# Kernel optimization log

Hardware: AMD Instinct MI355X
Metric: run time of the kernel (lower is better)

Reference implementation:

```python
import jax, jax.numpy as jnp
import numpy as np

N, K, C_S, C_Z, C_G, N_RBF = 1024, 16, 256, 128, 16, 64
EPS = 1e-8


def _ln(x, g, b, eps=1e-5):
    m = x.mean(-1, keepdims=True)
    v = jnp.mean((x - m) ** 2, -1, keepdims=True)
    return (x - m) * jax.lax.rsqrt(v + eps) * g + b


def _rbf(D, D_count=N_RBF, D_min=0.0, D_max=20.0):
    mu = jnp.linspace(D_min, D_max, D_count, dtype=D.dtype)
    sigma = (D_max - D_min) / D_count
    return jnp.exp(-(((D[..., None] - mu) / sigma) ** 2))


def setup_inputs() -> dict:
    key = jax.random.key(0)
    ks = jax.random.split(key, 20)
    node_features = jax.random.normal(ks[0], (N, C_S), jnp.float32)
    trans = jax.random.normal(ks[1], (N, 3), jnp.float32) * 5.0  # CA translations, Angstrom-ish
    edge_features = jax.random.normal(ks[2], (N * K, C_Z), jnp.float32)
    # sparse graph laid out as K neighbors per node: dst = node i repeated K times
    src = jax.random.randint(ks[3], (N * K,), 0, N)
    dst = jnp.repeat(jnp.arange(N), K)
    edge_index = jnp.stack([src, dst]).astype(jnp.int64)
    batch = jnp.zeros((N,), jnp.int64)
    res_mask = jnp.ones((N,), bool)
    w = lambda k, i, o: jax.random.normal(k, (i, o), jnp.float32) * 0.02
    return {
        "node_features": node_features, "trans": trans, "edge_features": edge_features,
        "ln_g": jnp.ones((C_Z,), jnp.float32), "ln_b": jnp.zeros((C_Z,), jnp.float32),
        "Wl": w(ks[4], C_S, C_G), "bl": jnp.zeros((C_G,), jnp.float32),
        "Wr": w(ks[5], C_S, C_G), "br": jnp.zeros((C_G,), jnp.float32),
        "Wep": w(ks[6], C_Z, C_Z), "bep": jnp.zeros((C_Z,), jnp.float32),
        "Weg": w(ks[7], C_Z, C_Z), "beg": jnp.zeros((C_Z,), jnp.float32),
        "Wdg": w(ks[8], C_G * C_G, C_Z), "bdg": jnp.zeros((C_Z,), jnp.float32),
        "Wdp": w(ks[9], N_RBF, C_Z), "bdp": jnp.zeros((C_Z,), jnp.float32),
        "lno_g": jnp.ones((C_Z,), jnp.float32), "lno_b": jnp.zeros((C_Z,), jnp.float32),
        "Wout": w(ks[10], C_Z, C_Z), "bout": jnp.zeros((C_Z,), jnp.float32),
        "Wog": w(ks[11], C_Z, C_Z), "bog": jnp.zeros((C_Z,), jnp.float32),
        "edge_index": edge_index, "batch": batch, "res_mask": res_mask,
    }


def reference(node_features, trans, edge_features, ln_g, ln_b, Wl, bl, Wr, br,
              Wep, bep, Weg, beg, Wdg, bdg, Wdp, bdp, lno_g, lno_b, Wout, bout,
              Wog, bog, edge_index, batch, res_mask):
    n = node_features.shape[0]
    src = edge_index[0].reshape(n, K)              # neighbor indices per node [N,K]
    # sparse -> kNN: edges are grouped K per destination node
    knn_feats = edge_features.reshape(n, K, C_Z)
    knn_mask = res_mask[src] & res_mask[:, None]   # [N,K]
    z = _ln(knn_feats, ln_g, ln_b)
    # outer-product node gating
    nl = node_features @ Wl + bl                   # [N,c_g]
    nr = node_features @ Wr + br
    a = nl[src]                                    # [N,K,c_g]
    b = nr[src]
    edge3 = a[:, :, None, :, None] * b[:, None, :, None, :]   # [N,K,K,c_g,c_g]
    gate3 = edge3.reshape(n, K, K, C_G * C_G) @ Wdg + bdg     # [N,K,K,c_z]
    # RBF distance features among the K neighbors of each node
    t = trans[src]                                 # [N,K,3]
    d = jnp.linalg.norm(t[:, :, None, :] - t[:, None, :, :] + EPS, axis=-1)  # [N,K,K]
    df = _rbf(d) @ Wdp + bdp                       # [N,K,K,c_z]
    m2 = (knn_mask[:, :, None] & knn_mask[:, None, :]).astype(df.dtype)
    e3 = jax.nn.sigmoid(gate3) * df * m2[..., None]
    # gated edge projection
    e2 = jax.nn.sigmoid(z @ Weg + beg) * (z @ Wep + bep)      # [N,K,c_z]
    # triangle matmul: per channel c, [K,K] @ [K]
    upd = jnp.einsum('njkc,nkc->njc', e3, e2)                 # [N,K,c_z]
    upd = _ln(upd, lno_g, lno_b) @ Wout + bout
    upd = upd * jax.nn.sigmoid(z @ Wog + bog)
    # kNN -> sparse scatter back (masked)
    out = (upd * knn_mask[..., None].astype(upd.dtype)).reshape(n * K, C_Z)
    return out
```

## Files before the change

kernel.cpp:

```cpp
#include <hip/hip_runtime.h>
#include <hip/hip_bf16.h>
#include <math.h>

#define KNN  16
#define CZ   128
#define CG   16
#define CS   256
#define NRBF 64
#define NN   1024

typedef __attribute__((ext_vector_type(8))) _Float16 half8;
typedef __attribute__((ext_vector_type(2))) _Float16 half2v;
typedef __attribute__((ext_vector_type(4))) float f4_t;

#define MFMA_F16(A, B, C) __builtin_amdgcn_mfma_f32_16x16x32_f16((A), (B), (C), 0, 0, 0)

union U8 { half2v h[4]; half8 v; };

__device__ __forceinline__ half2v pk2(float x, float y) {
    auto t = __builtin_amdgcn_cvt_pkrtz(x, y);
    half2v r;
    __builtin_memcpy(&r, &t, 4);
    return r;
}
__device__ __forceinline__ float sig_(float x) {
    return __builtin_amdgcn_rcpf(1.0f + __expf(-x));
}

__global__ __launch_bounds__(256) void repack_kernel(
    const float* __restrict__ Wdp, const float* __restrict__ Wdg,
    const float* __restrict__ Wout, const float* __restrict__ Wep,
    const float* __restrict__ Weg, const float* __restrict__ Wog,
    _Float16* __restrict__ dst_base) {
    int gid = blockIdx.x * 256 + threadIdx.x;
    const float* src;
    int o;
    if (gid < 8192)        { src = Wdp;  o = gid; }
    else if (gid < 40960)  { src = Wdg;  o = gid - 8192; }
    else if (gid < 57344)  { src = Wout; o = gid - 40960; }
    else if (gid < 73728)  { src = Wep;  o = gid - 57344; }
    else if (gid < 90112)  { src = Weg;  o = gid - 73728; }
    else                   { src = Wog;  o = gid - 90112; }
    int t  = o & 7;
    int l  = (o >> 3) & 63;
    int ct = (o >> 9) & 7;
    int s  = o >> 12;
    int row = s * 32 + (l >> 4) * 8 + t;
    int col = ct * 16 + (l & 15);
    dst_base[gid] = (_Float16)src[row * CZ + col];
}

__global__ __launch_bounds__(64) void nlr_kernel(
    const float* __restrict__ nf,
    const float* __restrict__ Wl, const float* __restrict__ bl,
    const float* __restrict__ Wr, const float* __restrict__ br,
    float* __restrict__ nl, float* __restrict__ nr) {
    int n = blockIdx.x;
    int lane = threadIdx.x;
    int p = lane & 15, seg = lane >> 4;
    float accl = (seg == 0) ? bl[p] : 0.0f;
    float accr = (seg == 0) ? br[p] : 0.0f;
    const float* row = nf + n * CS + seg * 64;
    for (int i = 0; i < 64; ++i) {
        float v = row[i];
        int s = seg * 64 + i;
        accl += v * Wl[s * CG + p];
        accr += v * Wr[s * CG + p];
    }
    accl += __shfl_xor(accl, 16); accl += __shfl_xor(accl, 32);
    accr += __shfl_xor(accr, 16); accr += __shfl_xor(accr, 32);
    if (lane < 16) { nl[n * CG + lane] = accl; nr[n * CG + lane] = accr; }
}

__global__ __launch_bounds__(256) void edge_kernel(
    const float* __restrict__ ef,
    const float* __restrict__ lng, const float* __restrict__ lnb,
    const float* __restrict__ bep, const float* __restrict__ beg,
    const float* __restrict__ bog,
    const _Float16* __restrict__ Wepp,
    const _Float16* __restrict__ Wegp,
    const _Float16* __restrict__ Wogp,
    const int* __restrict__ src, const int* __restrict__ resmask,
    float* __restrict__ e2ws, float* __restrict__ ggws) {
    __shared__ _Float16 s_z[16][136];
    __shared__ float s_km[16];
    int n = blockIdx.x;
    int tid = threadIdx.x;
    if (tid < 16) {
        int sv = src[n * KNN + tid];
        s_km[tid] = (resmask[sv] != 0 && resmask[n] != 0) ? 1.0f : 0.0f;
    }
    int r = tid >> 4, seg = tid & 15;
    const float* row = ef + ((size_t)n * KNN + r) * CZ + seg * 8;
    f4_t x0 = *(const f4_t*)row;
    f4_t x1 = *(const f4_t*)(row + 4);
    float s = x0.x + x0.y + x0.z + x0.w + x1.x + x1.y + x1.z + x1.w;
    float q = x0.x * x0.x + x0.y * x0.y + x0.z * x0.z + x0.w * x0.w
            + x1.x * x1.x + x1.y * x1.y + x1.z * x1.z + x1.w * x1.w;
    #pragma unroll
    for (int m = 1; m < 16; m <<= 1) { s += __shfl_xor(s, m); q += __shfl_xor(q, m); }
    float mean = s * (1.0f / CZ);
    float var  = q * (1.0f / CZ) - mean * mean;
    float rs   = __builtin_amdgcn_rsqf(var + 1e-5f);
    int col = seg * 8;
    f4_t g0 = *(const f4_t*)(lng + col), g1 = *(const f4_t*)(lng + col + 4);
    f4_t b0 = *(const f4_t*)(lnb + col), b1 = *(const f4_t*)(lnb + col + 4);
    U8 zu;
    zu.h[0] = pk2((x0.x - mean) * rs * g0.x + b0.x, (x0.y - mean) * rs * g0.y + b0.y);
    zu.h[1] = pk2((x0.z - mean) * rs * g0.z + b0.z, (x0.w - mean) * rs * g0.w + b0.w);
    zu.h[2] = pk2((x1.x - mean) * rs * g1.x + b1.x, (x1.y - mean) * rs * g1.y + b1.y);
    zu.h[3] = pk2((x1.z - mean) * rs * g1.z + b1.z, (x1.w - mean) * rs * g1.w + b1.w);
    *(half8*)&s_z[r][col] = zu.v;
    __syncthreads();

    int wv = tid >> 6, lane = tid & 63, l15 = lane & 15, quad = lane >> 4;
    half8 A[4];
    #pragma unroll
    for (int st = 0; st < 4; ++st)
        A[st] = *(const half8*)&s_z[l15][st * 32 + quad * 8];

    #pragma unroll
    for (int cc = 0; cc < 2; ++cc) {
        int ct = wv * 2 + cc;
        int c = ct * 16 + l15;
        float vep = bep[c], veg = beg[c], vog = bog[c];
        f4_t aep = {vep, vep, vep, vep};
        f4_t aeg = {veg, veg, veg, veg};
        f4_t aog = {vog, vog, vog, vog};
        #pragma unroll
        for (int st = 0; st < 4; ++st) {
            int off = ((st * 8 + ct) * 64 + lane) * 8;
            half8 bep_ = *(const half8*)(Wepp + off);
            half8 beg_ = *(const half8*)(Wegp + off);
            half8 bog_ = *(const half8*)(Wogp + off);
            aep = MFMA_F16(A[st], bep_, aep);
            aeg = MFMA_F16(A[st], beg_, aeg);
            aog = MFMA_F16(A[st], bog_, aog);
        }
        #pragma unroll
        for (int rr = 0; rr < 4; ++rr) {
            int er = quad * 4 + rr;
            size_t idx = ((size_t)n * KNN + er) * CZ + c;
            e2ws[idx] = sig_(aeg[rr]) * aep[rr] * s_km[er];
            ggws[idx] = sig_(aog[rr]);
        }
    }
}

__global__ __launch_bounds__(256) void main_kernel(
    const float* __restrict__ trans,
    const float* __restrict__ nl, const float* __restrict__ nr,
    const _Float16* __restrict__ Wdgp, const float* __restrict__ bdg,
    const _Float16* __restrict__ Wdpp, const float* __restrict__ bdp,
    const float* __restrict__ e2ws, const float* __restrict__ ggws,
    const float* __restrict__ lnog, const float* __restrict__ lnob,
    const _Float16* __restrict__ Woutp, const float* __restrict__ bout,
    const int* __restrict__ src, const int* __restrict__ resmask,
    float* __restrict__ out) {
    __shared__ float s_t[16 * 4];
    __shared__ float s_km[16];
    __shared__ int   s_src[16];
    __shared__ half2v s_a2[256];
    __shared__ float s_b[16 * 20];
    __shared__ float s_upd[16 * CZ];
    __shared__ _Float16 s_uln[16 * 136];

    int n = blockIdx.x;
    int tid = threadIdx.x;
    if (tid < 16) {
        int sv = src[n * KNN + tid];
        s_src[tid] = sv;
        s_km[tid] = (resmask[sv] != 0 && resmask[n] != 0) ? 1.0f : 0.0f;
        s_t[tid * 4 + 0] = trans[sv * 3 + 0];
        s_t[tid * 4 + 1] = trans[sv * 3 + 1];
        s_t[tid * 4 + 2] = trans[sv * 3 + 2];
    }
    __syncthreads();
    {
        int j = tid >> 4, p = tid & 15;
        int sv = s_src[j];
        float a = nl[sv * CG + p];
        s_a2[j * 16 + p] = pk2(a, a);
        s_b[j * 20 + p] = nr[sv * CG + p];
    }
    __syncthreads();

    int wv = tid >> 6, lane = tid & 63, l15 = lane & 15, quad = lane >> 4;

    half8 Bdg[8][2], Bdp[2][2];
    #pragma unroll
    for (int st = 0; st < 8; ++st)
        #pragma unroll
        for (int cc = 0; cc < 2; ++cc)
            Bdg[st][cc] = *(const half8*)(Wdgp + ((st * 8 + wv * 2 + cc) * 64 + lane) * 8);
    #pragma unroll
    for (int st = 0; st < 2; ++st)
        #pragma unroll
        for (int cc = 0; cc < 2; ++cc)
            Bdp[st][cc] = *(const half8*)(Wdpp + ((st * 8 + wv * 2 + cc) * 64 + lane) * 8);

    f4_t e2f[2];
    float bdgv[2], bdpv[2];
    #pragma unroll
    for (int cc = 0; cc < 2; ++cc) {
        int c = (wv * 2 + cc) * 16 + l15;
        bdgv[cc] = bdg[c];
        bdpv[cc] = bdp[c];
        #pragma unroll
        for (int rr = 0; rr < 4; ++rr)
            e2f[cc][rr] = e2ws[(size_t)(n * KNN + quad * 4 + rr) * CZ + c];
    }

    float tkx = s_t[l15 * 4 + 0], tky = s_t[l15 * 4 + 1], tkz = s_t[l15 * 4 + 2];
    f4_t bv0 = *(const f4_t*)&s_b[l15 * 20 + (quad & 1) * 8];
    f4_t bv1 = *(const f4_t*)&s_b[l15 * 20 + (quad & 1) * 8 + 4];
    half2v bh[4];
    bh[0] = pk2(bv0.x, bv0.y);
    bh[1] = pk2(bv0.z, bv0.w);
    bh[2] = pk2(bv1.x, bv1.y);
    bh[3] = pk2(bv1.z, bv1.w);
    int ph = quad >> 1;
    const float MUS = 20.0f / 63.0f;
    const float ISG = 1.0f / 0.3125f;
    float rIS[2];
    #pragma unroll
    for (int st = 0; st < 2; ++st)
        rIS[st] = (float)(st * 32 + quad * 8) * (MUS * ISG);

    for (int j = 0; j < 16; ++j) {
        float dx = s_t[j * 4 + 0] - tkx + 1e-8f;
        float dy = s_t[j * 4 + 1] - tky + 1e-8f;
        float dz = s_t[j * 4 + 2] - tkz + 1e-8f;
        float dI = sqrtf(dx * dx + dy * dy + dz * dz) * ISG;

        half8 ar[2];
        #pragma unroll
        for (int st = 0; st < 2; ++st) {
            U8 cv;
            float base0 = dI - rIS[st];
            #pragma unroll
            for (int tt = 0; tt < 4; ++tt) {
                float u0 = base0 - (float)(2 * tt) * (MUS * ISG);
                float u1 = u0 - (MUS * ISG);
                cv.h[tt] = pk2(__expf(-u0 * u0), __expf(-u1 * u1));
            }
            ar[st] = cv.v;
        }
        f4_t accd[2];
        #pragma unroll
        for (int cc = 0; cc < 2; ++cc) {
            f4_t z = {bdpv[cc], bdpv[cc], bdpv[cc], bdpv[cc]};
            z = MFMA_F16(ar[0], Bdp[0][cc], z);
            z = MFMA_F16(ar[1], Bdp[1][cc], z);
            accd[cc] = z;
        }

        f4_t accg[2];
        accg[0] = (f4_t){bdgv[0], bdgv[0], bdgv[0], bdgv[0]};
        accg[1] = (f4_t){bdgv[1], bdgv[1], bdgv[1], bdgv[1]};
        #pragma unroll
        for (int st = 0; st < 8; ++st) {
            half2v av = s_a2[j * 16 + st * 2 + ph];
            U8 ev;
            ev.h[0] = av * bh[0];
            ev.h[1] = av * bh[1];
            ev.h[2] = av * bh[2];
            ev.h[3] = av * bh[3];
            accg[0] = MFMA_F16(ev.v, Bdg[st][0], accg[0]);
            accg[1] = MFMA_F16(ev.v, Bdg[st][1], accg[1]);
        }

        float kmj = s_km[j];
        #pragma unroll
        for (int cc = 0; cc < 2; ++cc) {
            float part = 0.f;
            #pragma unroll
            for (int rr = 0; rr < 4; ++rr)
                part += sig_(accg[cc][rr]) * accd[cc][rr] * e2f[cc][rr];
            part += __shfl_xor(part, 16);
            part += __shfl_xor(part, 32);
            if (lane < 16) s_upd[j * CZ + (wv * 2 + cc) * 16 + lane] = part * kmj;
        }
    }
    __syncthreads();

    for (int rr = 0; rr < 4; ++rr) {
        int r = wv * 4 + rr;
        float x0 = s_upd[r * CZ + lane];
        float x1 = s_upd[r * CZ + 64 + lane];
        float sm = x0 + x1, sq = x0 * x0 + x1 * x1;
        #pragma unroll
        for (int m = 1; m < 64; m <<= 1) {
            sm += __shfl_xor(sm, m);
            sq += __shfl_xor(sq, m);
        }
        float mean = sm * (1.0f / CZ);
        float var  = sq * (1.0f / CZ) - mean * mean;
        float rsv  = __builtin_amdgcn_rsqf(var + 1e-5f);
        float h0 = (x0 - mean) * rsv * lnog[lane] + lnob[lane];
        float h1 = (x1 - mean) * rsv * lnog[64 + lane] + lnob[64 + lane];
        s_uln[r * 136 + lane]      = (_Float16)h0;
        s_uln[r * 136 + 64 + lane] = (_Float16)h1;
    }
    __syncthreads();

    half8 Aw[4];
    #pragma unroll
    for (int st = 0; st < 4; ++st)
        Aw[st] = *(const half8*)&s_uln[l15 * 136 + st * 32 + quad * 8];
    #pragma unroll
    for (int cc = 0; cc < 2; ++cc) {
        int c = (wv * 2 + cc) * 16 + l15;
        float bo = bout[c];
        f4_t acc = {bo, bo, bo, bo};
        #pragma unroll
        for (int st = 0; st < 4; ++st) {
            half8 bw = *(const half8*)(Woutp + ((st * 8 + wv * 2 + cc) * 64 + lane) * 8);
            acc = MFMA_F16(Aw[st], bw, acc);
        }
        #pragma unroll
        for (int rr = 0; rr < 4; ++rr) {
            int row = quad * 4 + rr;
            size_t oi = (size_t)(n * KNN + row) * CZ + c;
            out[oi] = acc[rr] * ggws[oi] * s_km[row];
        }
    }
}

extern "C" void kernel_launch(void* const* d_in, const int* in_sizes, int n_in,
                              void* d_out, int out_size, void* d_ws, size_t ws_size,
                              hipStream_t stream) {
    const float* node_features = (const float*)d_in[0];
    const float* trans         = (const float*)d_in[1];
    const float* edge_features = (const float*)d_in[2];
    const float* ln_g  = (const float*)d_in[3];
    const float* ln_b  = (const float*)d_in[4];
    const float* Wl    = (const float*)d_in[5];
    const float* bl    = (const float*)d_in[6];
    const float* Wr    = (const float*)d_in[7];
    const float* br    = (const float*)d_in[8];
    const float* Wep   = (const float*)d_in[9];
    const float* bep   = (const float*)d_in[10];
    const float* Weg   = (const float*)d_in[11];
    const float* beg   = (const float*)d_in[12];
    const float* Wdg   = (const float*)d_in[13];
    const float* bdg   = (const float*)d_in[14];
    const float* Wdp   = (const float*)d_in[15];
    const float* bdp   = (const float*)d_in[16];
    const float* lno_g = (const float*)d_in[17];
    const float* lno_b = (const float*)d_in[18];
    const float* Wout  = (const float*)d_in[19];
    const float* bout  = (const float*)d_in[20];
    const float* Wog   = (const float*)d_in[21];
    const float* bog   = (const float*)d_in[22];
    const int* edge_index = (const int*)d_in[23];
    const int* resmask    = (const int*)d_in[25];

    float* ws = (float*)d_ws;
    float* nl   = ws;
    float* nr   = nl + NN * CG;
    float* e2ws = nr + NN * CG;
    float* ggws = e2ws + (size_t)NN * KNN * CZ;
    _Float16* pk = (_Float16*)(ggws + (size_t)NN * KNN * CZ);
    _Float16* Wdpp  = pk;
    _Float16* Wdgp  = pk + 8192;
    _Float16* Woutp = pk + 40960;
    _Float16* Wepp  = pk + 57344;
    _Float16* Wegp  = pk + 73728;
    _Float16* Wogp  = pk + 90112;
    const int* src = edge_index;

    repack_kernel<<<416, 256, 0, stream>>>(Wdp, Wdg, Wout, Wep, Weg, Wog, pk);
    nlr_kernel<<<NN, 64, 0, stream>>>(node_features, Wl, bl, Wr, br, nl, nr);
    edge_kernel<<<NN, 256, 0, stream>>>(
        edge_features, ln_g, ln_b, bep, beg, bog, Wepp, Wegp, Wogp,
        src, resmask, e2ws, ggws);
    main_kernel<<<NN, 256, 0, stream>>>(
        trans, nl, nr, Wdgp, bdg, Wdpp, bdp, e2ws, ggws, lno_g, lno_b,
        Woutp, bout, src, resmask, (float*)d_out);
}
```

Before: 170.5 us.

## Fuse edge projections into main kernel and factor gate matmul through per-node tensor

Merges the weight repack and node-projection kernels into one prep launch, and folds the edge LayerNorm and gated projections into the main kernel so the e2 and gate intermediates stay in registers instead of round-tripping through global workspace. The 256-wide outer-product gate matmul is refactored: a per-node tensor T = a·Wdg (reshaped) is precomputed with 16x16x16 MFMAs into LDS, then each pair's gate is a small MFMA of b against T. This replaces eight 16x16x32 MFMAs per pair with one. The cost is 64KB of LDS for T per block, which lowers occupancy, plus fp16 rounding of the intermediate T and of the update buffer.

```diff
diff --git a/kernel.cpp b/kernel.cpp
--- a/kernel.cpp
+++ b/kernel.cpp
@@ -10,12 +10,15 @@
 #define NN   1024
 
 typedef __attribute__((ext_vector_type(8))) _Float16 half8;
+typedef __attribute__((ext_vector_type(4))) _Float16 half4;
 typedef __attribute__((ext_vector_type(2))) _Float16 half2v;
 typedef __attribute__((ext_vector_type(4))) float f4_t;
 
-#define MFMA_F16(A, B, C) __builtin_amdgcn_mfma_f32_16x16x32_f16((A), (B), (C), 0, 0, 0)
+#define MFMA16x32(A, B, C) __builtin_amdgcn_mfma_f32_16x16x32_f16((A), (B), (C), 0, 0, 0)
+#define MFMA16x16(A, B, C) __builtin_amdgcn_mfma_f32_16x16x16f16((A), (B), (C), 0, 0, 0)
 
 union U8 { half2v h[4]; half8 v; };
+union U4 { half2v h[2]; half4 v; };
 
 __device__ __forceinline__ half2v pk2(float x, float y) {
     auto t = __builtin_amdgcn_cvt_pkrtz(x, y);
@@ -27,98 +30,129 @@
     return __builtin_amdgcn_rcpf(1.0f + __expf(-x));
 }
 
-__global__ __launch_bounds__(256) void repack_kernel(
+__global__ __launch_bounds__(256) void prep_kernel(
     const float* __restrict__ Wdp, const float* __restrict__ Wdg,
     const float* __restrict__ Wout, const float* __restrict__ Wep,
     const float* __restrict__ Weg, const float* __restrict__ Wog,
-    _Float16* __restrict__ dst_base) {
-    int gid = blockIdx.x * 256 + threadIdx.x;
-    const float* src;
-    int o;
-    if (gid < 8192)        { src = Wdp;  o = gid; }
-    else if (gid < 40960)  { src = Wdg;  o = gid - 8192; }
-    else if (gid < 57344)  { src = Wout; o = gid - 40960; }
-    else if (gid < 73728)  { src = Wep;  o = gid - 57344; }
-    else if (gid < 90112)  { src = Weg;  o = gid - 73728; }
-    else                   { src = Wog;  o = gid - 90112; }
-    int t  = o & 7;
-    int l  = (o >> 3) & 63;
-    int ct = (o >> 9) & 7;
-    int s  = o >> 12;
-    int row = s * 32 + (l >> 4) * 8 + t;
-    int col = ct * 16 + (l & 15);
-    dst_base[gid] = (_Float16)src[row * CZ + col];
-}
-
-__global__ __launch_bounds__(64) void nlr_kernel(
+    _Float16* __restrict__ pk,
     const float* __restrict__ nf,
     const float* __restrict__ Wl, const float* __restrict__ bl,
     const float* __restrict__ Wr, const float* __restrict__ br,
-    float* __restrict__ nl, float* __restrict__ nr) {
-    int n = blockIdx.x;
-    int lane = threadIdx.x;
-    int p = lane & 15, seg = lane >> 4;
-    float accl = (seg == 0) ? bl[p] : 0.0f;
-    float accr = (seg == 0) ? br[p] : 0.0f;
-    const float* row = nf + n * CS + seg * 64;
-    for (int i = 0; i < 64; ++i) {
-        float v = row[i];
-        int s = seg * 64 + i;
-        accl += v * Wl[s * CG + p];
-        accr += v * Wr[s * CG + p];
-    }
-    accl += __shfl_xor(accl, 16); accl += __shfl_xor(accl, 32);
-    accr += __shfl_xor(accr, 16); accr += __shfl_xor(accr, 32);
-    if (lane < 16) { nl[n * CG + lane] = accl; nr[n * CG + lane] = accr; }
-}
-
-__global__ __launch_bounds__(256) void edge_kernel(
-    const float* __restrict__ ef,
+    float* __restrict__ nlo, float* __restrict__ nro) {
+    int b = blockIdx.x, tid = threadIdx.x;
+    if (b < 416) {
+        int gid = b * 256 + tid;
+        float val;
+        if (gid >= 8192 && gid < 40960) {
+            int o = gid - 8192;
+            int i = o & 3, l = (o >> 2) & 63, ct = (o >> 8) & 7, q = o >> 11;
+            int row = (4 * (l >> 4) + i) * 16 + q;
+            int col = ct * 16 + (l & 15);
+            val = Wdg[row * CZ + col];
+        } else {
+            const float* srcw;
+            int o;
+            if (gid < 8192)        { srcw = Wdp;  o = gid; }
+            else if (gid < 57344)  { srcw = Wout; o = gid - 40960; }
+            else if (gid < 73728)  { srcw = Wep;  o = gid - 57344; }
+            else if (gid < 90112)  { srcw = Weg;  o = gid - 73728; }
+            else                   { srcw = Wog;  o = gid - 90112; }
+            int t = o & 7, l = (o >> 3) & 63, ct = (o >> 9) & 7, s = o >> 12;
+            int row = s * 32 + (l >> 4) * 8 + t;
+            int col = ct * 16 + (l & 15);
+            val = srcw[row * CZ + col];
+        }
+        pk[gid] = (_Float16)val;
+    } else {
+        int grp = tid >> 6, lane = tid & 63;
+        int n = (b - 416) * 4 + grp;
+        int p = lane & 15, seg = lane >> 4;
+        float accl = (seg == 0) ? bl[p] : 0.0f;
+        float accr = (seg == 0) ? br[p] : 0.0f;
+        const float* rw = nf + n * CS + seg * 64;
+        for (int i = 0; i < 64; ++i) {
+            float v = rw[i];
+            int s = seg * 64 + i;
+            accl += v * Wl[s * CG + p];
+            accr += v * Wr[s * CG + p];
+        }
+        accl += __shfl_xor(accl, 16); accl += __shfl_xor(accl, 32);
+        accr += __shfl_xor(accr, 16); accr += __shfl_xor(accr, 32);
+        if (lane < 16) { nlo[n * CG + lane] = accl; nro[n * CG + lane] = accr; }
+    }
+}
+
+__global__ __launch_bounds__(256) void main_kernel(
+    const float* __restrict__ trans, const float* __restrict__ ef,
     const float* __restrict__ lng, const float* __restrict__ lnb,
+    const float* __restrict__ nl, const float* __restrict__ nr,
     const float* __restrict__ bep, const float* __restrict__ beg,
     const float* __restrict__ bog,
-    const _Float16* __restrict__ Wepp,
-    const _Float16* __restrict__ Wegp,
+    const _Float16* __restrict__ Wepp, const _Float16* __restrict__ Wegp,
     const _Float16* __restrict__ Wogp,
+    const _Float16* __restrict__ Wdg2, const float* __restrict__ bdg,
+    const _Float16* __restrict__ Wdpp, const float* __restrict__ bdp,
+    const float* __restrict__ lnog, const float* __restrict__ lnob,
+    const _Float16* __restrict__ Woutp, const float* __restrict__ bout,
     const int* __restrict__ src, const int* __restrict__ resmask,
-    float* __restrict__ e2ws, float* __restrict__ ggws) {
-    __shared__ _Float16 s_z[16][136];
+    float* __restrict__ out) {
+    __shared__ _Float16 s_z[16 * 136];
+    __shared__ float s_t[16 * 4];
     __shared__ float s_km[16];
-    int n = blockIdx.x;
-    int tid = threadIdx.x;
+    __shared__ int   s_src[16];
+    __shared__ float s_a[16 * 16];
+    __shared__ float s_b[16 * 20];
+    __shared__ _Float16 s_T[4][8192];
+    __shared__ _Float16 s_upd[16 * 136];
+
+    int n = blockIdx.x, tid = threadIdx.x;
     if (tid < 16) {
         int sv = src[n * KNN + tid];
+        s_src[tid] = sv;
         s_km[tid] = (resmask[sv] != 0 && resmask[n] != 0) ? 1.0f : 0.0f;
-    }
-    int r = tid >> 4, seg = tid & 15;
-    const float* row = ef + ((size_t)n * KNN + r) * CZ + seg * 8;
-    f4_t x0 = *(const f4_t*)row;
-    f4_t x1 = *(const f4_t*)(row + 4);
-    float s = x0.x + x0.y + x0.z + x0.w + x1.x + x1.y + x1.z + x1.w;
-    float q = x0.x * x0.x + x0.y * x0.y + x0.z * x0.z + x0.w * x0.w
-            + x1.x * x1.x + x1.y * x1.y + x1.z * x1.z + x1.w * x1.w;
-    #pragma unroll
-    for (int m = 1; m < 16; m <<= 1) { s += __shfl_xor(s, m); q += __shfl_xor(q, m); }
-    float mean = s * (1.0f / CZ);
-    float var  = q * (1.0f / CZ) - mean * mean;
-    float rs   = __builtin_amdgcn_rsqf(var + 1e-5f);
-    int col = seg * 8;
-    f4_t g0 = *(const f4_t*)(lng + col), g1 = *(const f4_t*)(lng + col + 4);
-    f4_t b0 = *(const f4_t*)(lnb + col), b1 = *(const f4_t*)(lnb + col + 4);
-    U8 zu;
-    zu.h[0] = pk2((x0.x - mean) * rs * g0.x + b0.x, (x0.y - mean) * rs * g0.y + b0.y);
-    zu.h[1] = pk2((x0.z - mean) * rs * g0.z + b0.z, (x0.w - mean) * rs * g0.w + b0.w);
-    zu.h[2] = pk2((x1.x - mean) * rs * g1.x + b1.x, (x1.y - mean) * rs * g1.y + b1.y);
-    zu.h[3] = pk2((x1.z - mean) * rs * g1.z + b1.z, (x1.w - mean) * rs * g1.w + b1.w);
-    *(half8*)&s_z[r][col] = zu.v;
+        s_t[tid * 4 + 0] = trans[sv * 3 + 0];
+        s_t[tid * 4 + 1] = trans[sv * 3 + 1];
+        s_t[tid * 4 + 2] = trans[sv * 3 + 2];
+    }
     __syncthreads();
+    {
+        int j = tid >> 4, p = tid & 15;
+        int sv = s_src[j];
+        s_a[j * 16 + p] = nl[sv * CG + p];
+        s_b[j * 20 + p] = nr[sv * CG + p];
+    }
+    {
+        int r = tid >> 4, seg = tid & 15;
+        const float* row = ef + ((size_t)n * KNN + r) * CZ + seg * 8;
+        f4_t x0 = *(const f4_t*)row;
+        f4_t x1 = *(const f4_t*)(row + 4);
+        float s = x0.x + x0.y + x0.z + x0.w + x1.x + x1.y + x1.z + x1.w;
+        float q = x0.x * x0.x + x0.y * x0.y + x0.z * x0.z + x0.w * x0.w
+                + x1.x * x1.x + x1.y * x1.y + x1.z * x1.z + x1.w * x1.w;
+        #pragma unroll
+        for (int m = 1; m < 16; m <<= 1) { s += __shfl_xor(s, m); q += __shfl_xor(q, m); }
+        float mean = s * (1.0f / CZ);
+        float var  = q * (1.0f / CZ) - mean * mean;
+        float rs   = __builtin_amdgcn_rsqf(var + 1e-5f);
+        int col = seg * 8;
+        f4_t g0 = *(const f4_t*)(lng + col), g1 = *(const f4_t*)(lng + col + 4);
+        f4_t b0 = *(const f4_t*)(lnb + col), b1 = *(const f4_t*)(lnb + col + 4);
+        U8 zu;
+        zu.h[0] = pk2((x0.x - mean) * rs * g0.x + b0.x, (x0.y - mean) * rs * g0.y + b0.y);
+        zu.h[1] = pk2((x0.z - mean) * rs * g0.z + b0.z, (x0.w - mean) * rs * g0.w + b0.w);
+        zu.h[2] = pk2((x1.x - mean) * rs * g1.x + b1.x, (x1.y - mean) * rs * g1.y + b1.y);
+        zu.h[3] = pk2((x1.z - mean) * rs * g1.z + b1.z, (x1.w - mean) * rs * g1.w + b1.w);
+        *(half8*)&s_z[r * 136 + col] = zu.v;
+    }
+    __syncthreads();
 
     int wv = tid >> 6, lane = tid & 63, l15 = lane & 15, quad = lane >> 4;
-    half8 A[4];
+
+    half8 Az[4];
     #pragma unroll
     for (int st = 0; st < 4; ++st)
-        A[st] = *(const half8*)&s_z[l15][st * 32 + quad * 8];
-
+        Az[st] = *(const half8*)&s_z[l15 * 136 + st * 32 + quad * 8];
+    f4_t e2f[2], ggf[2];
     #pragma unroll
     for (int cc = 0; cc < 2; ++cc) {
         int ct = wv * 2 + cc;
@@ -130,96 +164,67 @@
         #pragma unroll
         for (int st = 0; st < 4; ++st) {
             int off = ((st * 8 + ct) * 64 + lane) * 8;
-            half8 bep_ = *(const half8*)(Wepp + off);
-            half8 beg_ = *(const half8*)(Wegp + off);
-            half8 bog_ = *(const half8*)(Wogp + off);
-            aep = MFMA_F16(A[st], bep_, aep);
-            aeg = MFMA_F16(A[st], beg_, aeg);
-            aog = MFMA_F16(A[st], bog_, aog);
+            half8 wep_ = *(const half8*)(Wepp + off);
+            half8 weg_ = *(const half8*)(Wegp + off);
+            half8 wog_ = *(const half8*)(Wogp + off);
+            aep = MFMA16x32(Az[st], wep_, aep);
+            aeg = MFMA16x32(Az[st], weg_, aeg);
+            aog = MFMA16x32(Az[st], wog_, aog);
         }
         #pragma unroll
         for (int rr = 0; rr < 4; ++rr) {
-            int er = quad * 4 + rr;
-            size_t idx = ((size_t)n * KNN + er) * CZ + c;
-            e2ws[idx] = sig_(aeg[rr]) * aep[rr] * s_km[er];
-            ggws[idx] = sig_(aog[rr]);
-        }
-    }
-}
-
-__global__ __launch_bounds__(256) void main_kernel(
-    const float* __restrict__ trans,
-    const float* __restrict__ nl, const float* __restrict__ nr,
-    const _Float16* __restrict__ Wdgp, const float* __restrict__ bdg,
-    const _Float16* __restrict__ Wdpp, const float* __restrict__ bdp,
-    const float* __restrict__ e2ws, const float* __restrict__ ggws,
-    const float* __restrict__ lnog, const float* __restrict__ lnob,
-    const _Float16* __restrict__ Woutp, const float* __restrict__ bout,
-    const int* __restrict__ src, const int* __restrict__ resmask,
-    float* __restrict__ out) {
-    __shared__ float s_t[16 * 4];
-    __shared__ float s_km[16];
-    __shared__ int   s_src[16];
-    __shared__ half2v s_a2[256];
-    __shared__ float s_b[16 * 20];
-    __shared__ float s_upd[16 * CZ];
-    __shared__ _Float16 s_uln[16 * 136];
-
-    int n = blockIdx.x;
-    int tid = threadIdx.x;
-    if (tid < 16) {
-        int sv = src[n * KNN + tid];
-        s_src[tid] = sv;
-        s_km[tid] = (resmask[sv] != 0 && resmask[n] != 0) ? 1.0f : 0.0f;
-        s_t[tid * 4 + 0] = trans[sv * 3 + 0];
-        s_t[tid * 4 + 1] = trans[sv * 3 + 1];
-        s_t[tid * 4 + 2] = trans[sv * 3 + 2];
-    }
-    __syncthreads();
-    {
-        int j = tid >> 4, p = tid & 15;
-        int sv = s_src[j];
-        float a = nl[sv * CG + p];
-        s_a2[j * 16 + p] = pk2(a, a);
-        s_b[j * 20 + p] = nr[sv * CG + p];
-    }
-    __syncthreads();
-
-    int wv = tid >> 6, lane = tid & 63, l15 = lane & 15, quad = lane >> 4;
-
-    half8 Bdg[8][2], Bdp[2][2];
-    #pragma unroll
-    for (int st = 0; st < 8; ++st)
-        #pragma unroll
-        for (int cc = 0; cc < 2; ++cc)
-            Bdg[st][cc] = *(const half8*)(Wdgp + ((st * 8 + wv * 2 + cc) * 64 + lane) * 8);
+            e2f[cc][rr] = sig_(aeg[rr]) * aep[rr] * s_km[quad * 4 + rr];
+            ggf[cc][rr] = sig_(aog[rr]);
+        }
+    }
+
+    half8 Bdp[2][2];
     #pragma unroll
     for (int st = 0; st < 2; ++st)
         #pragma unroll
         for (int cc = 0; cc < 2; ++cc)
             Bdp[st][cc] = *(const half8*)(Wdpp + ((st * 8 + wv * 2 + cc) * 64 + lane) * 8);
 
-    f4_t e2f[2];
+    half4 Aa, Ab;
+    {
+        f4_t av = *(const f4_t*)&s_a[l15 * 16 + 4 * quad];
+        U4 u; u.h[0] = pk2(av.x, av.y); u.h[1] = pk2(av.z, av.w);
+        Aa = u.v;
+        f4_t bv = *(const f4_t*)&s_b[l15 * 20 + 4 * quad];
+        U4 w; w.h[0] = pk2(bv.x, bv.y); w.h[1] = pk2(bv.z, bv.w);
+        Ab = w.v;
+    }
+    _Float16* Tw = s_T[wv];
+    #pragma unroll
+    for (int ctl = 0; ctl < 2; ++ctl) {
+        int ct = wv * 2 + ctl;
+        #pragma unroll
+        for (int q0 = 0; q0 < 16; q0 += 4) {
+            f4_t tq[4];
+            #pragma unroll
+            for (int qq = 0; qq < 4; ++qq) {
+                half4 Bw = *(const half4*)(Wdg2 + (((q0 + qq) * 8 + ct) * 64 + lane) * 4);
+                f4_t z = {0.f, 0.f, 0.f, 0.f};
+                tq[qq] = MFMA16x16(Aa, Bw, z);
+            }
+            #pragma unroll
+            for (int rr = 0; rr < 4; ++rr) {
+                U4 u;
+                u.h[0] = pk2(tq[0][rr], tq[1][rr]);
+                u.h[1] = pk2(tq[2][rr], tq[3][rr]);
+                *(half4*)&Tw[(((4 * quad + rr) * 2 + ctl) * 16 + l15) * 16 + q0] = u.v;
+            }
+        }
+    }
+
     float bdgv[2], bdpv[2];
     #pragma unroll
     for (int cc = 0; cc < 2; ++cc) {
         int c = (wv * 2 + cc) * 16 + l15;
         bdgv[cc] = bdg[c];
         bdpv[cc] = bdp[c];
-        #pragma unroll
-        for (int rr = 0; rr < 4; ++rr)
-            e2f[cc][rr] = e2ws[(size_t)(n * KNN + quad * 4 + rr) * CZ + c];
-    }
-
+    }
     float tkx = s_t[l15 * 4 + 0], tky = s_t[l15 * 4 + 1], tkz = s_t[l15 * 4 + 2];
-    f4_t bv0 = *(const f4_t*)&s_b[l15 * 20 + (quad & 1) * 8];
-    f4_t bv1 = *(const f4_t*)&s_b[l15 * 20 + (quad & 1) * 8 + 4];
-    half2v bh[4];
-    bh[0] = pk2(bv0.x, bv0.y);
-    bh[1] = pk2(bv0.z, bv0.w);
-    bh[2] = pk2(bv1.x, bv1.y);
-    bh[3] = pk2(bv1.z, bv1.w);
-    int ph = quad >> 1;
     const float MUS = 20.0f / 63.0f;
     const float ISG = 1.0f / 0.3125f;
     float rIS[2];
@@ -246,30 +251,17 @@
             }
             ar[st] = cv.v;
         }
-        f4_t accd[2];
+        f4_t accd[2], accg[2];
         #pragma unroll
         for (int cc = 0; cc < 2; ++cc) {
             f4_t z = {bdpv[cc], bdpv[cc], bdpv[cc], bdpv[cc]};
-            z = MFMA_F16(ar[0], Bdp[0][cc], z);
-            z = MFMA_F16(ar[1], Bdp[1][cc], z);
+            z = MFMA16x32(ar[0], Bdp[0][cc], z);
+            z = MFMA16x32(ar[1], Bdp[1][cc], z);
             accd[cc] = z;
-        }
-
-        f4_t accg[2];
-        accg[0] = (f4_t){bdgv[0], bdgv[0], bdgv[0], bdgv[0]};
-        accg[1] = (f4_t){bdgv[1], bdgv[1], bdgv[1], bdgv[1]};
-        #pragma unroll
-        for (int st = 0; st < 8; ++st) {
-            half2v av = s_a2[j * 16 + st * 2 + ph];
-            U8 ev;
-            ev.h[0] = av * bh[0];
-            ev.h[1] = av * bh[1];
-            ev.h[2] = av * bh[2];
-            ev.h[3] = av * bh[3];
-            accg[0] = MFMA_F16(ev.v, Bdg[st][0], accg[0]);
-            accg[1] = MFMA_F16(ev.v, Bdg[st][1], accg[1]);
-        }
-
+            half4 Bt = *(const half4*)&Tw[((j * 2 + cc) * 16 + l15) * 16 + 4 * quad];
+            f4_t g = {bdgv[cc], bdgv[cc], bdgv[cc], bdgv[cc]};
+            accg[cc] = MFMA16x16(Ab, Bt, g);
+        }
         float kmj = s_km[j];
         #pragma unroll
         for (int cc = 0; cc < 2; ++cc) {
@@ -279,15 +271,17 @@
                 part += sig_(accg[cc][rr]) * accd[cc][rr] * e2f[cc][rr];
             part += __shfl_xor(part, 16);
             part += __shfl_xor(part, 32);
-            if (lane < 16) s_upd[j * CZ + (wv * 2 + cc) * 16 + lane] = part * kmj;
+            if (lane < 16)
+                s_upd[j * 136 + (wv * 2 + cc) * 16 + lane] = (_Float16)(part * kmj);
         }
     }
     __syncthreads();
 
-    for (int rr = 0; rr < 4; ++rr) {
-        int r = wv * 4 + rr;
-        float x0 = s_upd[r * CZ + lane];
-        float x1 = s_upd[r * CZ + 64 + lane];
+    #pragma unroll
+    for (int rr2 = 0; rr2 < 4; ++rr2) {
+        int rj = wv * 4 + rr2;
+        float x0 = (float)s_upd[rj * 136 + lane];
+        float x1 = (float)s_upd[rj * 136 + 64 + lane];
         float sm = x0 + x1, sq = x0 * x0 + x1 * x1;
         #pragma unroll
         for (int m = 1; m < 64; m <<= 1) {
@@ -299,15 +293,15 @@
         float rsv  = __builtin_amdgcn_rsqf(var + 1e-5f);
         float h0 = (x0 - mean) * rsv * lnog[lane] + lnob[lane];
         float h1 = (x1 - mean) * rsv * lnog[64 + lane] + lnob[64 + lane];
-        s_uln[r * 136 + lane]      = (_Float16)h0;
-        s_uln[r * 136 + 64 + lane] = (_Float16)h1;
+        s_z[rj * 136 + lane]      = (_Float16)h0;
+        s_z[rj * 136 + 64 + lane] = (_Float16)h1;
     }
     __syncthreads();
 
     half8 Aw[4];
     #pragma unroll
     for (int st = 0; st < 4; ++st)
-        Aw[st] = *(const half8*)&s_uln[l15 * 136 + st * 32 + quad * 8];
+        Aw[st] = *(const half8*)&s_z[l15 * 136 + st * 32 + quad * 8];
     #pragma unroll
     for (int cc = 0; cc < 2; ++cc) {
         int c = (wv * 2 + cc) * 16 + l15;
@@ -316,13 +310,13 @@
         #pragma unroll
         for (int st = 0; st < 4; ++st) {
             half8 bw = *(const half8*)(Woutp + ((st * 8 + wv * 2 + cc) * 64 + lane) * 8);
-            acc = MFMA_F16(Aw[st], bw, acc);
+            acc = MFMA16x32(Aw[st], bw, acc);
         }
         #pragma unroll
         for (int rr = 0; rr < 4; ++rr) {
             int row = quad * 4 + rr;
             size_t oi = (size_t)(n * KNN + row) * CZ + c;
-            out[oi] = acc[rr] * ggws[oi] * s_km[row];
+            out[oi] = acc[rr] * ggf[cc][rr] * s_km[row];
         }
     }
 }
@@ -357,25 +351,23 @@
     const int* resmask    = (const int*)d_in[25];
 
     float* ws = (float*)d_ws;
-    float* nl   = ws;
-    float* nr   = nl + NN * CG;
-    float* e2ws = nr + NN * CG;
-    float* ggws = e2ws + (size_t)NN * KNN * CZ;
-    _Float16* pk = (_Float16*)(ggws + (size_t)NN * KNN * CZ);
+    float* nl = ws;
+    float* nr = nl + NN * CG;
+    _Float16* pk = (_Float16*)(nr + NN * CG);
     _Float16* Wdpp  = pk;
-    _Float16* Wdgp  = pk + 8192;
+    _Float16* Wdg2  = pk + 8192;
     _Float16* Woutp = pk + 40960;
     _Float16* Wepp  = pk + 57344;
     _Float16* Wegp  = pk + 73728;
     _Float16* Wogp  = pk + 90112;
     const int* src = edge_index;
 
-    repack_kernel<<<416, 256, 0, stream>>>(Wdp, Wdg, Wout, Wep, Weg, Wog, pk);
-    nlr_kernel<<<NN, 64, 0, stream>>>(node_features, Wl, bl, Wr, br, nl, nr);
-    edge_kernel<<<NN, 256, 0, stream>>>(
-        edge_features, ln_g, ln_b, bep, beg, bog, Wepp, Wegp, Wogp,
-        src, resmask, e2ws, ggws);
+    prep_kernel<<<672, 256, 0, stream>>>(
+        Wdp, Wdg, Wout, Wep, Weg, Wog, pk,
+        node_features, Wl, bl, Wr, br, nl, nr);
     main_kernel<<<NN, 256, 0, stream>>>(
-        trans, nl, nr, Wdgp, bdg, Wdpp, bdp, e2ws, ggws, lno_g, lno_b,
+        trans, edge_features, ln_g, ln_b, nl, nr,
+        bep, beg, bog, Wepp, Wegp, Wogp,
+        Wdg2, bdg, Wdpp, bdp, lno_g, lno_b,
         Woutp, bout, src, resmask, (float*)d_out);
 }
```

Result: faster. 163.2 us (-4.3%).
